# Performance work log

Measured on AMD Instinct MI355X. Metric: run time of the kernel, lower is better.

The kernel has to match this reference:

```python
import jax, jax.numpy as jnp
import numpy as np

SEGMENT_LENGTHS = (2048, 4096, 8192)
DILATION_RATES = (1, 2, 4)
NUM_HEADS = 12
EMBED_DIM = 768
B, N = 2, 8192


def setup_inputs() -> dict:
    key = jax.random.key(0)
    ks = jax.random.split(key, 11)
    E = EMBED_DIM
    return {
        "query": jax.random.normal(ks[0], (B, N, E), jnp.float32),
        "key": jax.random.normal(ks[1], (B, N, E), jnp.float32),
        "value": jax.random.normal(ks[2], (B, N, E), jnp.float32),
        "Wq": jax.random.normal(ks[3], (E, E), jnp.float32) * (E ** -0.5),
        "bq": jax.random.normal(ks[4], (E,), jnp.float32) * 0.02,
        "Wk": jax.random.normal(ks[5], (E, E), jnp.float32) * (E ** -0.5),
        "bk": jax.random.normal(ks[6], (E,), jnp.float32) * 0.02,
        "Wv": jax.random.normal(ks[7], (E, E), jnp.float32) * (E ** -0.5),
        "bv": jax.random.normal(ks[8], (E,), jnp.float32) * 0.02,
        "Wo": jax.random.normal(ks[9], (E, E), jnp.float32) * (E ** -0.5),
        "bo": jax.random.normal(ks[10], (E,), jnp.float32) * 0.02,
    }


def _dilated_attention(q, k, v):
    # q, k, v: [b, n, h, d]
    b, n, h, d = q.shape
    num_groups = len(DILATION_RATES)
    g = h // num_groups  # heads per dilation group
    scale = float(1.0 / np.sqrt(d))  # xformers default softmax scale
    out = jnp.zeros_like(q)
    for i, (r, s) in enumerate(zip(DILATION_RATES, SEGMENT_LENGTHS)):
        off = i % r
        hmin, hmax = i * g, (i + 1) * g
        nseg = n // s
        # gather: [b, nseg, s/r, g, d]
        qg = q.reshape(b, nseg, s, h, d)[:, :, off::r, hmin:hmax, :]
        kg = k.reshape(b, nseg, s, h, d)[:, :, off::r, hmin:hmax, :]
        vg = v.reshape(b, nseg, s, h, d)[:, :, off::r, hmin:hmax, :]
        scores = jnp.einsum("bnqhd,bnkhd->bnhqk", qg, kg) * scale
        attn = jax.nn.softmax(scores, axis=-1)
        x = jnp.einsum("bnhqk,bnkhd->bnqhd", attn, vg)
        out = (
            out.reshape(b, nseg, s, h, d)
            .at[:, :, off::r, hmin:hmax, :]
            .add(x)
            .reshape(b, n, h, d)
        )
    # faithful to original: normalize by sum over the sequence dimension
    return out / jnp.sum(out, axis=1, keepdims=True)


def reference(query, key, value, Wq, bq, Wk, bk, Wv, bv, Wo, bo):
    b, n, e = query.shape
    h = NUM_HEADS
    d = e // h
    q = (query @ Wq.T + bq).reshape(b, n, h, d)
    k = (key @ Wk.T + bk).reshape(b, n, h, d)
    v = (value @ Wv.T + bv).reshape(b, n, h, d)
    x = _dilated_attention(q, k, v)
    x = x.reshape(b, n, e)
    return x @ Wo.T + bo
```

## Files before the change

### kernel.cpp

```cpp
#include <hip/hip_runtime.h>
#include <hip/hip_bf16.h>
#include <cmath>
#include <cstdint>

#define B_ 2
#define N_ 8192
#define H_ 12
#define D_ 64
#define E_ 768
#define M_ (B_*N_)

typedef __attribute__((ext_vector_type(8))) short short8;
typedef __attribute__((ext_vector_type(4))) short short4v;
typedef __attribute__((ext_vector_type(4))) float float4v;

__device__ inline short f2b(float f) {
  union { float f; unsigned u; } x; x.f = f;
  unsigned r = (x.u + 0x7fffu + ((x.u >> 16) & 1u)) >> 16;
  return (short)r;
}
__device__ inline float b2f(short s) {
  union { unsigned u; float f; } x; x.u = ((unsigned)(unsigned short)s) << 16;
  return x.f;
}
__device__ inline void split2(float f, short& h, short& l) {
  h = f2b(f);
  l = f2b(f - b2f(h));
}
__device__ inline unsigned pack_trunc(float a, float b) {
  return (__float_as_uint(b) & 0xffff0000u) | (__float_as_uint(a) >> 16);
}

#define MFMA(a, b, c) __builtin_amdgcn_mfma_f32_16x16x32_bf16((a), (b), (c), 0, 0, 0)

#define GLOAD_LDS16(g, l) \
  __builtin_amdgcn_global_load_lds((const __attribute__((address_space(1))) void*)(g), \
      (__attribute__((address_space(3))) void*)(l), 16, 0, 0)

__global__ __launch_bounds__(256) void split_kernel(const float* __restrict__ src,
    short* __restrict__ hi, short* __restrict__ lo, int count4)
{
  int i = blockIdx.x * 256 + threadIdx.x;
  if (i >= count4) return;
  float4v t = ((const float4v*)src)[i];
  short4v h4, l4; short hh, ll;
  split2(t.x, hh, ll); h4.x = hh; l4.x = ll;
  split2(t.y, hh, ll); h4.y = hh; l4.y = ll;
  split2(t.z, hh, ll); h4.z = hh; l4.z = ll;
  split2(t.w, hh, ll); h4.w = hh; l4.w = ll;
  ((short4v*)hi)[i] = h4;
  ((short4v*)lo)[i] = l4;
}

__global__ __launch_bounds__(256) void split_w4(
    const float* __restrict__ w0, const float* __restrict__ w1,
    const float* __restrict__ w2, const float* __restrict__ w3,
    short* __restrict__ planes)
{
  int which = blockIdx.y;
  const float* src = which == 0 ? w0 : which == 1 ? w1 : which == 2 ? w2 : w3;
  short* hi = planes + (size_t)(2 * which) * (E_ * E_);
  short* lo = planes + (size_t)(2 * which + 1) * (E_ * E_);
  int i = blockIdx.x * 256 + threadIdx.x;
  if (i >= E_ * E_ / 4) return;
  float4v t = ((const float4v*)src)[i];
  short4v h4, l4; short hh, ll;
  split2(t.x, hh, ll); h4.x = hh; l4.x = ll;
  split2(t.y, hh, ll); h4.y = hh; l4.y = ll;
  split2(t.z, hh, ll); h4.z = hh; l4.z = ll;
  split2(t.w, hh, ll); h4.w = hh; l4.w = ll;
  ((short4v*)hi)[i] = h4;
  ((short4v*)lo)[i] = l4;
}

__global__ __launch_bounds__(256) void inv_kernel(const float* __restrict__ sums,
    float* __restrict__ inv)
{
  int i = blockIdx.x * 256 + threadIdx.x;
  if (i < B_ * E_) inv[i] = 1.0f / sums[i];
}

__global__ __launch_bounds__(256) void prep_out(const float* __restrict__ attn,
    const float* __restrict__ inv, short* __restrict__ xnh, short* __restrict__ xnl)
{
  size_t e4 = ((size_t)blockIdx.x * 256 + threadIdx.x) * 4;
  int e = (int)(e4 % E_);
  int b = (int)(e4 / ((size_t)E_ * N_));
  float4v a = *(const float4v*)(attn + e4);
  float4v iv = *(const float4v*)(inv + (size_t)b * E_ + e);
  a *= iv;
  short4v h4, l4; short hh, ll;
  split2(a.x, hh, ll); h4.x = hh; l4.x = ll;
  split2(a.y, hh, ll); h4.y = hh; l4.y = ll;
  split2(a.z, hh, ll); h4.z = hh; l4.z = ll;
  split2(a.w, hh, ll); h4.w = hh; l4.w = ll;
  *(short4v*)&xnh[e4] = h4;
  *(short4v*)&xnl[e4] = l4;
}

template<bool OUT_PAIR>
__global__ __launch_bounds__(256) void gemm_dma(
    const short* __restrict__ Ah, const short* __restrict__ Al,
    const short* __restrict__ Wh, const short* __restrict__ Wl,
    const float* __restrict__ bias, void* __restrict__ OutH, short* __restrict__ OutL)
{
  __shared__ short Ash[4096], Asl[4096], Wsh[4096], Wsl[4096];
  const int tid = threadIdx.x;
  const int m0 = blockIdx.y * 128;
  const int n0 = blockIdx.x * 128;
  const int w = tid >> 6, lane = tid & 63, quad = lane >> 4, l16 = lane & 15;
  const int wr = w >> 1, wc = w & 1;
  const int cq = (l16 >> 1) & 3;
  const int dmarow = lane >> 2;
  const int dmacc = (((lane & 3) ^ ((lane >> 3) & 3))) * 8;

  float4v acc[4][4];
#pragma unroll
  for (int a = 0; a < 4; ++a)
#pragma unroll
    for (int c = 0; c < 4; ++c) acc[a][c] = (float4v)0.0f;

  for (int kt = 0; kt < 24; ++kt) {
    const int k0 = kt * 32;
#pragma unroll
    for (int i = 0; i < 2; ++i) {
      int c = w * 2 + i;
      int ldso = c * 512 + lane * 8;
      size_t ga = (size_t)(m0 + c * 16 + dmarow) * E_ + k0 + dmacc;
      size_t gw = (size_t)(n0 + c * 16 + dmarow) * E_ + k0 + dmacc;
      GLOAD_LDS16(Ah + ga, &Ash[ldso]);
      GLOAD_LDS16(Al + ga, &Asl[ldso]);
      GLOAD_LDS16(Wh + gw, &Wsh[ldso]);
      GLOAD_LDS16(Wl + gw, &Wsl[ldso]);
    }
    __syncthreads();

    short8 afh[4], afl[4], bfh[4], bfl[4];
#pragma unroll
    for (int rt = 0; rt < 4; ++rt) {
      int ao = (wr * 64 + rt * 16 + l16) * 32 + (quad ^ cq) * 8;
      afh[rt] = *(const short8*)&Ash[ao];
      afl[rt] = *(const short8*)&Asl[ao];
      int wo = (wc * 64 + rt * 16 + l16) * 32 + (quad ^ cq) * 8;
      bfh[rt] = *(const short8*)&Wsh[wo];
      bfl[rt] = *(const short8*)&Wsl[wo];
    }
#pragma unroll
    for (int rt = 0; rt < 4; ++rt)
#pragma unroll
      for (int ct = 0; ct < 4; ++ct) {
        float4v a = acc[rt][ct];
        a = MFMA(afh[rt], bfh[ct], a);
        a = MFMA(afh[rt], bfl[ct], a);
        a = MFMA(afl[rt], bfh[ct], a);
        acc[rt][ct] = a;
      }
    __syncthreads();
  }

#pragma unroll
  for (int ct = 0; ct < 4; ++ct) {
    int n = n0 + wc * 64 + ct * 16 + l16;
    float bv = bias[n];
#pragma unroll
    for (int rt = 0; rt < 4; ++rt) {
#pragma unroll
      for (int i = 0; i < 4; ++i) {
        int m = m0 + wr * 64 + rt * 16 + quad * 4 + i;
        float v = acc[rt][ct][i] + bv;
        if constexpr (OUT_PAIR) {
          short hh, ll; split2(v, hh, ll);
          ((short*)OutH)[(size_t)m * E_ + n] = hh;
          OutL[(size_t)m * E_ + n] = ll;
        } else {
          ((float*)OutH)[(size_t)m * E_ + n] = v;
        }
      }
    }
  }
}

__device__ __host__ inline int hoff_of(int g, int hg) {
  return g == 0 ? hg * 8192 : (g == 1 ? 32768 + hg * 4096 : 49152 + hg * 2048);
}

__global__ __launch_bounds__(256) void transpose_v(const short* __restrict__ vh,
    const short* __restrict__ vl, short* __restrict__ vgh, short* __restrict__ vgl)
{
  __shared__ short Lh[64 * 68], Ll[64 * 68];
  int bid = blockIdx.x;
  int b = 0;
  if (bid >= 896) { b = 1; bid -= 896; }
  int g, hg, tile;
  if (bid < 512)      { g = 0; hg = bid >> 7; tile = bid & 127; }
  else if (bid < 768) { g = 1; hg = (bid - 512) >> 6; tile = (bid - 512) & 63; }
  else                { g = 2; hg = (bid - 768) >> 5; tile = (bid - 768) & 31; }
  const int h = g * 4 + hg, r = 1 << g, off = g;
  const int ext = 8192 >> g;
  const int jj0 = tile * 64, seg = jj0 >> 11, j0 = jj0 & 2047;
  const int n0 = seg * (2048 << g) + off + j0 * r;
  const int tid = threadIdx.x;

#pragma unroll
  for (int p = 0; p < 2; ++p) {
    int c = tid + p * 256;
    int jr = c >> 3, c8 = (c & 7) * 8;
    size_t gsrc = ((size_t)(b * N_ + n0 + jr * r) * H_ + h) * D_ + c8;
    *(short8*)&Lh[jr * 68 + c8] = *(const short8*)(vh + gsrc);
    *(short8*)&Ll[jr * 68 + c8] = *(const short8*)(vl + gsrc);
  }
  __syncthreads();
  size_t basebh = ((size_t)b * 57344 + hoff_of(g, hg)) * 64;
#pragma unroll
  for (int p = 0; p < 2; ++p) {
    int c = tid + p * 256;
    int dd = c >> 3, jc = (c & 7) * 8;
    short8 oh, ol;
#pragma unroll
    for (int u = 0; u < 8; ++u) {
      oh[u] = Lh[(jc + u) * 68 + dd];
      ol[u] = Ll[(jc + u) * 68 + dd];
    }
    size_t gdst = basebh + (size_t)dd * ext + jj0 + jc;
    *(short8*)(vgh + gdst) = oh;
    *(short8*)(vgl + gdst) = ol;
  }
}

__global__ __launch_bounds__(256) void attn_kernel(
    const short* __restrict__ qh, const short* __restrict__ ql,
    const short* __restrict__ kh, const short* __restrict__ kl,
    const short* __restrict__ vgh, const short* __restrict__ vgl,
    float* __restrict__ attn_out, float* __restrict__ sums)
{
  __shared__ short Ksh[32 * 72], Ksl[32 * 72];
  __shared__ short Vth[64 * 40], Vtl[64 * 40];
  __shared__ short Psh[4][32 * 40], Psl[4][32 * 40];

  int bid = blockIdx.x;
  int g, t;
  if (bid < 512)      { g = 0; t = bid; }
  else if (bid < 768) { g = 1; t = bid - 512; }
  else                { g = 2; t = bid - 768; }
  const int qtile = t & 15; t >>= 4;
  const int hg = t & 3; t >>= 2;
  const int nseg = 4 >> g;
  const int seg = t & (nseg - 1);
  const int b = t / nseg;
  const int r = 1 << g;
  const int off = g;
  const int h = g * 4 + hg;
  const int segbase = seg * (2048 << g);
  const int ext = 8192 >> g;

  const int tid = threadIdx.x;
  const int w = tid >> 6, lane = tid & 63, quad = lane >> 4, l16 = lane & 15;

  const size_t vbase = ((size_t)b * 57344 + hoff_of(g, hg)) * 64 + (size_t)seg * 2048;

  if (g > 0) {
#pragma unroll
    for (int res0 = 1; res0 < 4; ++res0) {
      if (res0 >= r) break;
      int res = (off + res0) & (r - 1);
      for (int c = 0; c < 8; ++c) {
        int idx = tid + c * 256;
        int jl = idx >> 4, d0 = (idx & 15) * 4;
        int pos = segbase + res + (qtile * 128 + jl) * r;
        *(float4v*)(attn_out + ((size_t)(b * N_ + pos) * H_ + h) * D_ + d0) = (float4v)0.f;
      }
    }
  }

  short8 qfh[2][2], qfl[2][2];
#pragma unroll
  for (int qt = 0; qt < 2; ++qt) {
    int j = qtile * 128 + w * 32 + qt * 16 + l16;
    int pos = segbase + off + j * r;
    size_t base = ((size_t)(b * N_ + pos) * H_ + h) * D_;
#pragma unroll
    for (int ks = 0; ks < 2; ++ks) {
      qfh[qt][ks] = *(const short8*)(qh + base + ks * 32 + quad * 8);
      qfl[qt][ks] = *(const short8*)(ql + base + ks * 32 + quad * 8);
    }
  }

  float4v o[4][2];
  float mrow[2], lrow[2];
#pragma unroll
  for (int dt = 0; dt < 4; ++dt)
#pragma unroll
    for (int qt = 0; qt < 2; ++qt) o[dt][qt] = (float4v)0.0f;
  mrow[0] = mrow[1] = -INFINITY;
  lrow[0] = lrow[1] = 0.f;

  for (int kt = 0; kt < 64; ++kt) {
    {
      int row = tid >> 3, c8 = (tid & 7) * 8;
      int posk = segbase + off + (kt * 32 + row) * r;
      size_t gb = ((size_t)(b * N_ + posk) * H_ + h) * D_ + c8;
      *(short8*)&Ksh[row * 72 + c8] = *(const short8*)(kh + gb);
      *(short8*)&Ksl[row * 72 + c8] = *(const short8*)(kl + gb);
      int dd = tid >> 2, kvc = (tid & 3) * 8;
      size_t vb = vbase + (size_t)dd * ext + kt * 32 + kvc;
      *(short8*)&Vth[dd * 40 + kvc] = *(const short8*)(vgh + vb);
      *(short8*)&Vtl[dd * 40 + kvc] = *(const short8*)(vgl + vb);
    }
    __syncthreads();

    float4v sc[2][2];
#pragma unroll
    for (int kvt = 0; kvt < 2; ++kvt) {
      const int kb = (kvt * 16 + l16) * 72 + quad * 8;
      short8 ah0 = *(const short8*)&Ksh[kb];
      short8 ah1 = *(const short8*)&Ksh[kb + 32];
      short8 al0 = *(const short8*)&Ksl[kb];
      short8 al1 = *(const short8*)&Ksl[kb + 32];
#pragma unroll
      for (int qt = 0; qt < 2; ++qt) {
        float4v a = (float4v)0.0f;
        a = MFMA(ah0, qfh[qt][0], a); a = MFMA(ah1, qfh[qt][1], a);
        a = MFMA(ah0, qfl[qt][0], a); a = MFMA(ah1, qfl[qt][1], a);
        a = MFMA(al0, qfh[qt][0], a); a = MFMA(al1, qfh[qt][1], a);
        sc[qt][kvt] = a * 0.125f;
      }
    }

#pragma unroll
    for (int qt = 0; qt < 2; ++qt) {
      float mx = sc[qt][0][0];
#pragma unroll
      for (int kvt = 0; kvt < 2; ++kvt)
#pragma unroll
        for (int i = 0; i < 4; ++i) mx = fmaxf(mx, sc[qt][kvt][i]);
      mx = fmaxf(mx, __shfl_xor(mx, 16, 64));
      mx = fmaxf(mx, __shfl_xor(mx, 32, 64));
      if (__any(mx > mrow[qt])) {
        float mnew = fmaxf(mrow[qt], mx);
        float alpha = __expf(mrow[qt] - mnew);
        mrow[qt] = mnew;
        lrow[qt] *= alpha;
#pragma unroll
        for (int dt = 0; dt < 4; ++dt) o[dt][qt] *= alpha;
      }
      float rs = 0.f;
#pragma unroll
      for (int kvt = 0; kvt < 2; ++kvt)
#pragma unroll
        for (int i = 0; i < 4; ++i) {
          float p = __expf(sc[qt][kvt][i] - mrow[qt]);
          sc[qt][kvt][i] = p;
          rs += p;
        }
      rs += __shfl_xor(rs, 16, 64);
      rs += __shfl_xor(rs, 32, 64);
      lrow[qt] += rs;

#pragma unroll
      for (int kvt = 0; kvt < 2; ++kvt)
#pragma unroll
        for (int c = 0; c < 2; ++c) {
          float pa = sc[qt][kvt][2 * c], pb = sc[qt][kvt][2 * c + 1];
          unsigned ua = __float_as_uint(pa), ub = __float_as_uint(pb);
          float la = pa - __uint_as_float(ua & 0xffff0000u);
          float lb = pb - __uint_as_float(ub & 0xffff0000u);
          int ad = (qt * 16 + l16) * 40 + kvt * 16 + quad * 4 + 2 * c;
          *(unsigned*)&Psh[w][ad] = (ub & 0xffff0000u) | (ua >> 16);
          *(unsigned*)&Psl[w][ad] = pack_trunc(la, lb);
        }
    }

    short8 pfh[2], pfl[2];
#pragma unroll
    for (int qt = 0; qt < 2; ++qt) {
      pfh[qt] = *(const short8*)&Psh[w][(qt * 16 + l16) * 40 + quad * 8];
      pfl[qt] = *(const short8*)&Psl[w][(qt * 16 + l16) * 40 + quad * 8];
    }
#pragma unroll
    for (int dt = 0; dt < 4; ++dt) {
      short8 vfh = *(const short8*)&Vth[(dt * 16 + l16) * 40 + quad * 8];
      short8 vfl = *(const short8*)&Vtl[(dt * 16 + l16) * 40 + quad * 8];
#pragma unroll
      for (int qt = 0; qt < 2; ++qt) {
        float4v a = o[dt][qt];
        a = MFMA(vfh, pfh[qt], a);
        a = MFMA(vfh, pfl[qt], a);
        a = MFMA(vfl, pfh[qt], a);
        o[dt][qt] = a;
      }
    }
    __syncthreads();
  }

  float4v sacc[4];
#pragma unroll
  for (int dt = 0; dt < 4; ++dt) sacc[dt] = (float4v)0.0f;
#pragma unroll
  for (int qt = 0; qt < 2; ++qt) {
    float inv_l = 1.0f / lrow[qt];
    int j = qtile * 128 + w * 32 + qt * 16 + l16;
    int pos = segbase + off + j * r;
    float* dst = attn_out + ((size_t)(b * N_ + pos) * H_ + h) * D_;
#pragma unroll
    for (int dt = 0; dt < 4; ++dt) {
      float4v v = o[dt][qt] * inv_l;
      *(float4v*)(dst + dt * 16 + quad * 4) = v;
      sacc[dt] += v;
    }
  }
#pragma unroll
  for (int dt = 0; dt < 4; ++dt) {
#pragma unroll
    for (int i = 0; i < 4; ++i) {
      float x = sacc[dt][i];
      x += __shfl_xor(x, 1, 64);
      x += __shfl_xor(x, 2, 64);
      x += __shfl_xor(x, 4, 64);
      x += __shfl_xor(x, 8, 64);
      if (l16 == 0)
        atomicAdd(&sums[(size_t)b * E_ + h * D_ + dt * 16 + quad * 4 + i], x);
    }
  }
}

extern "C" void kernel_launch(void* const* d_in, const int* in_sizes, int n_in,
                              void* d_out, int out_size, void* d_ws, size_t ws_size,
                              hipStream_t stream)
{
  const float* query = (const float*)d_in[0];
  const float* key_  = (const float*)d_in[1];
  const float* value = (const float*)d_in[2];
  const float* Wq = (const float*)d_in[3];
  const float* bq = (const float*)d_in[4];
  const float* Wk = (const float*)d_in[5];
  const float* bk = (const float*)d_in[6];
  const float* Wv = (const float*)d_in[7];
  const float* bv = (const float*)d_in[8];
  const float* Wo = (const float*)d_in[9];
  const float* bo = (const float*)d_in[10];

  char* ws = (char*)d_ws;
  const size_t szbf = (size_t)M_ * E_ * 2;
  const size_t szvg = (size_t)2 * 57344 * 64 * 2;
  const size_t szw  = (size_t)E_ * E_ * 2;
  short* qh_ = (short*)(ws);
  short* ql_ = (short*)(ws + 1 * szbf);
  short* kh_ = (short*)(ws + 2 * szbf);
  short* kl_ = (short*)(ws + 3 * szbf);
  short* vh_ = (short*)(ws + 4 * szbf);
  short* vl_ = (short*)(ws + 5 * szbf);
  short* ish = (short*)(ws + 6 * szbf);
  short* isl = (short*)(ws + 7 * szbf);
  short* vgh = (short*)(ws + 6 * szbf);
  short* vgl = (short*)(ws + 6 * szbf + szvg);
  short* wsp = (short*)(ws + 8 * szbf);
  float* sums = (float*)(ws + 8 * szbf + 8 * szw);
  float* attn = (float*)(ws + 4 * szbf);
  float* inv  = (float*)qh_;
  short* xnh = kh_;
  short* xnl = kl_;
  short* wqh = wsp + 0 * (szw / 2), *wql = wsp + 1 * (szw / 2);
  short* wkh = wsp + 2 * (szw / 2), *wkl = wsp + 3 * (szw / 2);
  short* wvh = wsp + 4 * (szw / 2), *wvl = wsp + 5 * (szw / 2);
  short* woh = wsp + 6 * (szw / 2), *wol = wsp + 7 * (szw / 2);

  hipMemsetAsync(sums, 0, (size_t)B_ * E_ * sizeof(float), stream);

  split_w4<<<dim3(576, 4), 256, 0, stream>>>(Wq, Wk, Wv, Wo, wsp);

  const int ac4 = M_ * E_ / 4;
  dim3 gg(6, 128), gb(256);
  split_kernel<<<12288, 256, 0, stream>>>(query, ish, isl, ac4);
  gemm_dma<true><<<gg, gb, 0, stream>>>(ish, isl, wqh, wql, bq, qh_, ql_);
  split_kernel<<<12288, 256, 0, stream>>>(key_, ish, isl, ac4);
  gemm_dma<true><<<gg, gb, 0, stream>>>(ish, isl, wkh, wkl, bk, kh_, kl_);
  split_kernel<<<12288, 256, 0, stream>>>(value, ish, isl, ac4);
  gemm_dma<true><<<gg, gb, 0, stream>>>(ish, isl, wvh, wvl, bv, vh_, vl_);

  transpose_v<<<1792, 256, 0, stream>>>(vh_, vl_, vgh, vgl);
  attn_kernel<<<896, 256, 0, stream>>>(qh_, ql_, kh_, kl_, vgh, vgl, attn, sums);
  inv_kernel<<<6, 256, 0, stream>>>(sums, inv);
  prep_out<<<12288, 256, 0, stream>>>(attn, inv, xnh, xnl);
  gemm_dma<false><<<gg, gb, 0, stream>>>(xnh, xnl, woh, wol, bo, d_out, nullptr);
}
```

Baseline: 879.8 us.

## Double-buffer K/V tiles with register prefetch and shuffle P via bpermute

The attention kernel now double-buffers K and V tiles in shared memory and prefetches the next-next tile into registers, so global loads overlap with the MFMA work instead of stalling before each iteration. The P-matrix round trip through per-wave shared memory is replaced with ds_bpermute lane shuffles. The scale now folds in log2(e) so exp2f can be used, and s_setprio is raised around the MFMA blocks. These changes add register pressure, and the launch bounds are tightened to request 4 blocks per SM. The loop's final iterations prefetch wrapped tiles (index mod 64), which are loaded but never used.

After: 879.2 us. About the same (-0.1%).

```diff
diff --git a/kernel.cpp b/kernel.cpp
--- a/kernel.cpp
+++ b/kernel.cpp
@@ -227,15 +227,14 @@
   }
 }
 
-__global__ __launch_bounds__(256) void attn_kernel(
+__global__ __launch_bounds__(256, 4) void attn_kernel(
     const short* __restrict__ qh, const short* __restrict__ ql,
     const short* __restrict__ kh, const short* __restrict__ kl,
     const short* __restrict__ vgh, const short* __restrict__ vgl,
     float* __restrict__ attn_out, float* __restrict__ sums)
 {
-  __shared__ short Ksh[32 * 72], Ksl[32 * 72];
-  __shared__ short Vth[64 * 40], Vtl[64 * 40];
-  __shared__ short Psh[4][32 * 40], Psl[4][32 * 40];
+  __shared__ __align__(16) short Ksh[2][32 * 72], Ksl[2][32 * 72];
+  __shared__ __align__(16) short Vth[2][64 * 40], Vtl[2][64 * 40];
 
   int bid = blockIdx.x;
   int g, t;
@@ -255,6 +254,9 @@
 
   const int tid = threadIdx.x;
   const int w = tid >> 6, lane = tid & 63, quad = lane >> 4, l16 = lane & 15;
+  const bool hi5 = (lane & 32) != 0;
+  const int addrA = (l16 + ((lane >> 4) & 1) * 32) << 2;
+  const int addrB = addrA + 64;
 
   const size_t vbase = ((size_t)b * 57344 + hoff_of(g, hg)) * 64 + (size_t)seg * 2048;
 
@@ -285,6 +287,26 @@
     }
   }
 
+  const int srow = tid >> 3, sc8 = (tid & 7) * 8;
+  const int sdd = tid >> 2, skvc = (tid & 3) * 8;
+  size_t gbK = ((size_t)(b * N_ + segbase + off + srow * r) * H_ + h) * D_ + sc8;
+  const size_t stepK = (size_t)32 * r * (H_ * D_);
+  size_t gbV = vbase + (size_t)sdd * ext + skvc;
+
+  short8 rkh, rkl, rvh, rvl;
+#define LOADT(tt) do { \
+    size_t ka_ = gbK + (size_t)(tt) * stepK; \
+    size_t va_ = gbV + (size_t)(tt) * 32; \
+    rkh = *(const short8*)(kh + ka_); rkl = *(const short8*)(kl + ka_); \
+    rvh = *(const short8*)(vgh + va_); rvl = *(const short8*)(vgl + va_); \
+  } while (0)
+#define WRITET(cc) do { \
+    *(short8*)&Ksh[cc][srow * 72 + sc8] = rkh; \
+    *(short8*)&Ksl[cc][srow * 72 + sc8] = rkl; \
+    *(short8*)&Vth[cc][sdd * 40 + skvc] = rvh; \
+    *(short8*)&Vtl[cc][sdd * 40 + skvc] = rvl; \
+  } while (0)
+
   float4v o[4][2];
   float mrow[2], lrow[2];
 #pragma unroll
@@ -294,50 +316,51 @@
   mrow[0] = mrow[1] = -INFINITY;
   lrow[0] = lrow[1] = 0.f;
 
+  LOADT(0);
+  WRITET(0);
+  LOADT(1);
+  __syncthreads();
+  int cur = 0;
+
   for (int kt = 0; kt < 64; ++kt) {
-    {
-      int row = tid >> 3, c8 = (tid & 7) * 8;
-      int posk = segbase + off + (kt * 32 + row) * r;
-      size_t gb = ((size_t)(b * N_ + posk) * H_ + h) * D_ + c8;
-      *(short8*)&Ksh[row * 72 + c8] = *(const short8*)(kh + gb);
-      *(short8*)&Ksl[row * 72 + c8] = *(const short8*)(kl + gb);
-      int dd = tid >> 2, kvc = (tid & 3) * 8;
-      size_t vb = vbase + (size_t)dd * ext + kt * 32 + kvc;
-      *(short8*)&Vth[dd * 40 + kvc] = *(const short8*)(vgh + vb);
-      *(short8*)&Vtl[dd * 40 + kvc] = *(const short8*)(vgl + vb);
-    }
-    __syncthreads();
+    WRITET(cur ^ 1);
+    LOADT((kt + 2) & 63);
+
+    const short* Kc_h = Ksh[cur]; const short* Kc_l = Ksl[cur];
+    const short* Vc_h = Vth[cur]; const short* Vc_l = Vtl[cur];
 
     float4v sc[2][2];
+    __builtin_amdgcn_s_setprio(1);
 #pragma unroll
     for (int kvt = 0; kvt < 2; ++kvt) {
       const int kb = (kvt * 16 + l16) * 72 + quad * 8;
-      short8 ah0 = *(const short8*)&Ksh[kb];
-      short8 ah1 = *(const short8*)&Ksh[kb + 32];
-      short8 al0 = *(const short8*)&Ksl[kb];
-      short8 al1 = *(const short8*)&Ksl[kb + 32];
+      short8 ah0 = *(const short8*)&Kc_h[kb];
+      short8 ah1 = *(const short8*)&Kc_h[kb + 32];
+      short8 al0 = *(const short8*)&Kc_l[kb];
+      short8 al1 = *(const short8*)&Kc_l[kb + 32];
 #pragma unroll
       for (int qt = 0; qt < 2; ++qt) {
         float4v a = (float4v)0.0f;
         a = MFMA(ah0, qfh[qt][0], a); a = MFMA(ah1, qfh[qt][1], a);
         a = MFMA(ah0, qfl[qt][0], a); a = MFMA(ah1, qfl[qt][1], a);
         a = MFMA(al0, qfh[qt][0], a); a = MFMA(al1, qfh[qt][1], a);
-        sc[qt][kvt] = a * 0.125f;
-      }
-    }
-
+        sc[qt][kvt] = a * 0.18033688f;
+      }
+    }
+    __builtin_amdgcn_s_setprio(0);
+
+    short8 pfh[2], pfl[2];
 #pragma unroll
     for (int qt = 0; qt < 2; ++qt) {
-      float mx = sc[qt][0][0];
-#pragma unroll
-      for (int kvt = 0; kvt < 2; ++kvt)
-#pragma unroll
-        for (int i = 0; i < 4; ++i) mx = fmaxf(mx, sc[qt][kvt][i]);
+      float mx = fmaxf(fmaxf(fmaxf(sc[qt][0][0], sc[qt][0][1]),
+                             fmaxf(sc[qt][0][2], sc[qt][0][3])),
+                       fmaxf(fmaxf(sc[qt][1][0], sc[qt][1][1]),
+                             fmaxf(sc[qt][1][2], sc[qt][1][3])));
       mx = fmaxf(mx, __shfl_xor(mx, 16, 64));
       mx = fmaxf(mx, __shfl_xor(mx, 32, 64));
       if (__any(mx > mrow[qt])) {
         float mnew = fmaxf(mrow[qt], mx);
-        float alpha = __expf(mrow[qt] - mnew);
+        float alpha = exp2f(mrow[qt] - mnew);
         mrow[qt] = mnew;
         lrow[qt] *= alpha;
 #pragma unroll
@@ -348,7 +371,7 @@
       for (int kvt = 0; kvt < 2; ++kvt)
 #pragma unroll
         for (int i = 0; i < 4; ++i) {
-          float p = __expf(sc[qt][kvt][i] - mrow[qt]);
+          float p = exp2f(sc[qt][kvt][i] - mrow[qt]);
           sc[qt][kvt][i] = p;
           rs += p;
         }
@@ -356,30 +379,40 @@
       rs += __shfl_xor(rs, 32, 64);
       lrow[qt] += rs;
 
+      unsigned wv_h[2][2], wv_l[2][2];
 #pragma unroll
       for (int kvt = 0; kvt < 2; ++kvt)
 #pragma unroll
         for (int c = 0; c < 2; ++c) {
           float pa = sc[qt][kvt][2 * c], pb = sc[qt][kvt][2 * c + 1];
           unsigned ua = __float_as_uint(pa), ub = __float_as_uint(pb);
+          wv_h[kvt][c] = (ub & 0xffff0000u) | (ua >> 16);
           float la = pa - __uint_as_float(ua & 0xffff0000u);
           float lb = pb - __uint_as_float(ub & 0xffff0000u);
-          int ad = (qt * 16 + l16) * 40 + kvt * 16 + quad * 4 + 2 * c;
-          *(unsigned*)&Psh[w][ad] = (ub & 0xffff0000u) | (ua >> 16);
-          *(unsigned*)&Psl[w][ad] = pack_trunc(la, lb);
+          wv_l[kvt][c] = pack_trunc(la, lb);
         }
-    }
-
-    short8 pfh[2], pfl[2];
-#pragma unroll
-    for (int qt = 0; qt < 2; ++qt) {
-      pfh[qt] = *(const short8*)&Psh[w][(qt * 16 + l16) * 40 + quad * 8];
-      pfl[qt] = *(const short8*)&Psl[w][(qt * 16 + l16) * 40 + quad * 8];
-    }
+      union { unsigned u[4]; short8 s; } oh, ol;
+#pragma unroll
+      for (int j = 0; j < 4; ++j) {
+        int ad = (j < 2) ? addrA : addrB;
+        int c = j & 1;
+        unsigned h0 = (unsigned)__builtin_amdgcn_ds_bpermute(ad, (int)wv_h[0][c]);
+        unsigned h1 = (unsigned)__builtin_amdgcn_ds_bpermute(ad, (int)wv_h[1][c]);
+        unsigned l0 = (unsigned)__builtin_amdgcn_ds_bpermute(ad, (int)wv_l[0][c]);
+        unsigned l1 = (unsigned)__builtin_amdgcn_ds_bpermute(ad, (int)wv_l[1][c]);
+        oh.u[j] = hi5 ? h1 : h0;
+        ol.u[j] = hi5 ? l1 : l0;
+      }
+      pfh[qt] = oh.s;
+      pfl[qt] = ol.s;
+    }
+
+    __builtin_amdgcn_s_setprio(1);
 #pragma unroll
     for (int dt = 0; dt < 4; ++dt) {
-      short8 vfh = *(const short8*)&Vth[(dt * 16 + l16) * 40 + quad * 8];
-      short8 vfl = *(const short8*)&Vtl[(dt * 16 + l16) * 40 + quad * 8];
+      const int vo = (dt * 16 + l16) * 40 + quad * 8;
+      short8 vfh = *(const short8*)&Vc_h[vo];
+      short8 vfl = *(const short8*)&Vc_l[vo];
 #pragma unroll
       for (int qt = 0; qt < 2; ++qt) {
         float4v a = o[dt][qt];
@@ -389,8 +422,13 @@
         o[dt][qt] = a;
       }
     }
+    __builtin_amdgcn_s_setprio(0);
+
     __syncthreads();
-  }
+    cur ^= 1;
+  }
+#undef LOADT
+#undef WRITET
 
   float4v sacc[4];
 #pragma unroll
```

## Software-pipeline attention loop with double-buffered K/V and register-permuted P

Applied to the files above, without the earlier changes.

Restructures the attention inner loop into a two-stage software pipeline. K and V tiles are double-buffered in shared memory and prefetched through registers, and the QK^T of the next tile overlaps the softmax and PV of the current one. P is moved to MFMA operand layout with ds_bpermute instead of a shared-memory round trip. The softmax scale times log2(e) is folded into the Q projection epilogue so exp2f can be used, the row-sum reduction is deferred to the end, and blocks are remapped across groups. It also adds launch bounds and setprio hints, at the cost of more register pressure and more complex control flow.

After: 1.155 ms. +31.2%, slower.

```diff
diff --git a/kernel.cpp b/kernel.cpp
--- a/kernel.cpp
+++ b/kernel.cpp
@@ -102,7 +102,8 @@
 __global__ __launch_bounds__(256) void gemm_dma(
     const short* __restrict__ Ah, const short* __restrict__ Al,
     const short* __restrict__ Wh, const short* __restrict__ Wl,
-    const float* __restrict__ bias, void* __restrict__ OutH, short* __restrict__ OutL)
+    const float* __restrict__ bias, void* __restrict__ OutH, short* __restrict__ OutL,
+    float oscale)
 {
   __shared__ short Ash[4096], Asl[4096], Wsh[4096], Wsl[4096];
   const int tid = threadIdx.x;
@@ -167,7 +168,7 @@
 #pragma unroll
       for (int i = 0; i < 4; ++i) {
         int m = m0 + wr * 64 + rt * 16 + quad * 4 + i;
-        float v = acc[rt][ct][i] + bv;
+        float v = (acc[rt][ct][i] + bv) * oscale;
         if constexpr (OUT_PAIR) {
           short hh, ll; split2(v, hh, ll);
           ((short*)OutH)[(size_t)m * E_ + n] = hh;
@@ -227,17 +228,16 @@
   }
 }
 
-__global__ __launch_bounds__(256) void attn_kernel(
+__global__ __launch_bounds__(256, 4) void attn_kernel(
     const short* __restrict__ qh, const short* __restrict__ ql,
     const short* __restrict__ kh, const short* __restrict__ kl,
     const short* __restrict__ vgh, const short* __restrict__ vgl,
     float* __restrict__ attn_out, float* __restrict__ sums)
 {
-  __shared__ short Ksh[32 * 72], Ksl[32 * 72];
-  __shared__ short Vth[64 * 40], Vtl[64 * 40];
-  __shared__ short Psh[4][32 * 40], Psl[4][32 * 40];
-
-  int bid = blockIdx.x;
+  __shared__ __align__(16) short Ksh[2][32 * 72], Ksl[2][32 * 72];
+  __shared__ __align__(16) short Vth[2][64 * 40], Vtl[2][64 * 40];
+
+  int bid = (blockIdx.x & 7) * 112 + (blockIdx.x >> 3);
   int g, t;
   if (bid < 512)      { g = 0; t = bid; }
   else if (bid < 768) { g = 1; t = bid - 512; }
@@ -255,6 +255,9 @@
 
   const int tid = threadIdx.x;
   const int w = tid >> 6, lane = tid & 63, quad = lane >> 4, l16 = lane & 15;
+  const bool hi5 = (lane & 32) != 0;
+  const int addrA = (l16 + ((lane >> 4) & 1) * 32) << 2;
+  const int addrB = addrA + 64;
 
   const size_t vbase = ((size_t)b * 57344 + hoff_of(g, hg)) * 64 + (size_t)seg * 2048;
 
@@ -285,6 +288,111 @@
     }
   }
 
+  const int srow = tid >> 3, sc8 = (tid & 7) * 8;
+  const int sdd = tid >> 2, skvc = (tid & 3) * 8;
+  size_t gbK = ((size_t)(b * N_ + segbase + off + srow * r) * H_ + h) * D_ + sc8;
+  const size_t stepK = (size_t)32 * r * (H_ * D_);
+  size_t gbV = vbase + (size_t)sdd * ext + skvc;
+
+  short8 rkh, rkl, rvh, rvl;
+#define TCLAMP(tt) ((tt) > 63 ? 63 : (tt))
+#define LOADK(tt) do { size_t ka_ = gbK + (size_t)(tt) * stepK; \
+    rkh = *(const short8*)(kh + ka_); rkl = *(const short8*)(kl + ka_); } while (0)
+#define LOADV(tt) do { size_t va_ = gbV + (size_t)(tt) * 32; \
+    rvh = *(const short8*)(vgh + va_); rvl = *(const short8*)(vgl + va_); } while (0)
+#define WRITEK(cc) do { *(short8*)&Ksh[cc][srow * 72 + sc8] = rkh; \
+    *(short8*)&Ksl[cc][srow * 72 + sc8] = rkl; } while (0)
+#define WRITEV(cc) do { *(short8*)&Vth[cc][sdd * 40 + skvc] = rvh; \
+    *(short8*)&Vtl[cc][sdd * 40 + skvc] = rvl; } while (0)
+
+#define QK_INTO(sdst, kbuf) do { \
+    __builtin_amdgcn_s_setprio(1); \
+    _Pragma("unroll") \
+    for (int kvt = 0; kvt < 2; ++kvt) { \
+      const int kb = (kvt * 16 + l16) * 72 + quad * 8; \
+      short8 ah0 = *(const short8*)&Ksh[kbuf][kb]; \
+      short8 ah1 = *(const short8*)&Ksh[kbuf][kb + 32]; \
+      short8 al0 = *(const short8*)&Ksl[kbuf][kb]; \
+      short8 al1 = *(const short8*)&Ksl[kbuf][kb + 32]; \
+      _Pragma("unroll") \
+      for (int qt = 0; qt < 2; ++qt) { \
+        float4v a = (float4v)0.0f; \
+        a = MFMA(ah0, qfh[qt][0], a); a = MFMA(ah1, qfh[qt][1], a); \
+        a = MFMA(ah0, qfl[qt][0], a); a = MFMA(ah1, qfl[qt][1], a); \
+        a = MFMA(al0, qfh[qt][0], a); a = MFMA(al1, qfh[qt][1], a); \
+        sdst[qt][kvt] = a; \
+      } \
+    } \
+    __builtin_amdgcn_s_setprio(0); \
+  } while (0)
+
+#define SOFTMAX_PV(s, vv) do { \
+    short8 pfh[2], pfl[2]; \
+    _Pragma("unroll") \
+    for (int qt = 0; qt < 2; ++qt) { \
+      float mx = fmaxf(fmaxf(fmaxf(s[qt][0][0], s[qt][0][1]), \
+                             fmaxf(s[qt][0][2], s[qt][0][3])), \
+                       fmaxf(fmaxf(s[qt][1][0], s[qt][1][1]), \
+                             fmaxf(s[qt][1][2], s[qt][1][3]))); \
+      mx = fmaxf(mx, __shfl_xor(mx, 16, 64)); \
+      mx = fmaxf(mx, __shfl_xor(mx, 32, 64)); \
+      if (__any(mx > mrow[qt])) { \
+        float mnew = fmaxf(mrow[qt], mx); \
+        float alpha = exp2f(mrow[qt] - mnew); \
+        mrow[qt] = mnew; lrow[qt] *= alpha; \
+        _Pragma("unroll") for (int dt = 0; dt < 4; ++dt) o[dt][qt] *= alpha; \
+      } \
+      float rs = 0.f; \
+      _Pragma("unroll") \
+      for (int kvt = 0; kvt < 2; ++kvt) \
+        _Pragma("unroll") \
+        for (int i = 0; i < 4; ++i) { \
+          float p = exp2f(s[qt][kvt][i] - mrow[qt]); \
+          s[qt][kvt][i] = p; rs += p; \
+        } \
+      lrow[qt] += rs;   \
+      unsigned wv_h[2][2], wv_l[2][2]; \
+      _Pragma("unroll") \
+      for (int kvt = 0; kvt < 2; ++kvt) \
+        _Pragma("unroll") \
+        for (int c = 0; c < 2; ++c) { \
+          float pa = s[qt][kvt][2 * c], pb = s[qt][kvt][2 * c + 1]; \
+          unsigned ua = __float_as_uint(pa), ub = __float_as_uint(pb); \
+          wv_h[kvt][c] = (ub & 0xffff0000u) | (ua >> 16); \
+          float la = pa - __uint_as_float(ua & 0xffff0000u); \
+          float lb = pb - __uint_as_float(ub & 0xffff0000u); \
+          wv_l[kvt][c] = pack_trunc(la, lb); \
+        } \
+      union { unsigned u[4]; short8 sv; } oh_, ol_; \
+      _Pragma("unroll") \
+      for (int j = 0; j < 4; ++j) { \
+        int ad = (j < 2) ? addrA : addrB; int c = j & 1; \
+        unsigned h0 = (unsigned)__builtin_amdgcn_ds_bpermute(ad, (int)wv_h[0][c]); \
+        unsigned h1 = (unsigned)__builtin_amdgcn_ds_bpermute(ad, (int)wv_h[1][c]); \
+        unsigned l0 = (unsigned)__builtin_amdgcn_ds_bpermute(ad, (int)wv_l[0][c]); \
+        unsigned l1 = (unsigned)__builtin_amdgcn_ds_bpermute(ad, (int)wv_l[1][c]); \
+        oh_.u[j] = hi5 ? h1 : h0; ol_.u[j] = hi5 ? l1 : l0; \
+      } \
+      pfh[qt] = oh_.sv; pfl[qt] = ol_.sv; \
+    } \
+    __builtin_amdgcn_s_setprio(1); \
+    _Pragma("unroll") \
+    for (int dt = 0; dt < 4; ++dt) { \
+      const int vo = (dt * 16 + l16) * 40 + quad * 8; \
+      short8 vfh = *(const short8*)&Vth[vv][vo]; \
+      short8 vfl = *(const short8*)&Vtl[vv][vo]; \
+      _Pragma("unroll") \
+      for (int qt = 0; qt < 2; ++qt) { \
+        float4v a = o[dt][qt]; \
+        a = MFMA(vfh, pfh[qt], a); \
+        a = MFMA(vfh, pfl[qt], a); \
+        a = MFMA(vfl, pfh[qt], a); \
+        o[dt][qt] = a; \
+      } \
+    } \
+    __builtin_amdgcn_s_setprio(0); \
+  } while (0)
+
   float4v o[4][2];
   float mrow[2], lrow[2];
 #pragma unroll
@@ -294,109 +402,47 @@
   mrow[0] = mrow[1] = -INFINITY;
   lrow[0] = lrow[1] = 0.f;
 
-  for (int kt = 0; kt < 64; ++kt) {
-    {
-      int row = tid >> 3, c8 = (tid & 7) * 8;
-      int posk = segbase + off + (kt * 32 + row) * r;
-      size_t gb = ((size_t)(b * N_ + posk) * H_ + h) * D_ + c8;
-      *(short8*)&Ksh[row * 72 + c8] = *(const short8*)(kh + gb);
-      *(short8*)&Ksl[row * 72 + c8] = *(const short8*)(kl + gb);
-      int dd = tid >> 2, kvc = (tid & 3) * 8;
-      size_t vb = vbase + (size_t)dd * ext + kt * 32 + kvc;
-      *(short8*)&Vth[dd * 40 + kvc] = *(const short8*)(vgh + vb);
-      *(short8*)&Vtl[dd * 40 + kvc] = *(const short8*)(vgl + vb);
-    }
+  float4v sA[2][2], sB[2][2];
+
+  LOADK(0); LOADV(0);
+  WRITEK(0); WRITEV(0);
+  LOADK(1);
+  __syncthreads();
+  WRITEK(1);
+  QK_INTO(sA, 0);
+  LOADK(2); LOADV(1);
+  __syncthreads();
+
+  for (int u = 0; u < 32; ++u) {
+    const int kt = 2 * u;
+    WRITEK(0);
+    WRITEV(1);
+    LOADK(TCLAMP(kt + 3)); LOADV(TCLAMP(kt + 2));
+    QK_INTO(sB, 1);
+    SOFTMAX_PV(sA, 0);
     __syncthreads();
-
-    float4v sc[2][2];
-#pragma unroll
-    for (int kvt = 0; kvt < 2; ++kvt) {
-      const int kb = (kvt * 16 + l16) * 72 + quad * 8;
-      short8 ah0 = *(const short8*)&Ksh[kb];
-      short8 ah1 = *(const short8*)&Ksh[kb + 32];
-      short8 al0 = *(const short8*)&Ksl[kb];
-      short8 al1 = *(const short8*)&Ksl[kb + 32];
-#pragma unroll
-      for (int qt = 0; qt < 2; ++qt) {
-        float4v a = (float4v)0.0f;
-        a = MFMA(ah0, qfh[qt][0], a); a = MFMA(ah1, qfh[qt][1], a);
-        a = MFMA(ah0, qfl[qt][0], a); a = MFMA(ah1, qfl[qt][1], a);
-        a = MFMA(al0, qfh[qt][0], a); a = MFMA(al1, qfh[qt][1], a);
-        sc[qt][kvt] = a * 0.125f;
-      }
-    }
-
-#pragma unroll
-    for (int qt = 0; qt < 2; ++qt) {
-      float mx = sc[qt][0][0];
-#pragma unroll
-      for (int kvt = 0; kvt < 2; ++kvt)
-#pragma unroll
-        for (int i = 0; i < 4; ++i) mx = fmaxf(mx, sc[qt][kvt][i]);
-      mx = fmaxf(mx, __shfl_xor(mx, 16, 64));
-      mx = fmaxf(mx, __shfl_xor(mx, 32, 64));
-      if (__any(mx > mrow[qt])) {
-        float mnew = fmaxf(mrow[qt], mx);
-        float alpha = __expf(mrow[qt] - mnew);
-        mrow[qt] = mnew;
-        lrow[qt] *= alpha;
-#pragma unroll
-        for (int dt = 0; dt < 4; ++dt) o[dt][qt] *= alpha;
-      }
-      float rs = 0.f;
-#pragma unroll
-      for (int kvt = 0; kvt < 2; ++kvt)
-#pragma unroll
-        for (int i = 0; i < 4; ++i) {
-          float p = __expf(sc[qt][kvt][i] - mrow[qt]);
-          sc[qt][kvt][i] = p;
-          rs += p;
-        }
-      rs += __shfl_xor(rs, 16, 64);
-      rs += __shfl_xor(rs, 32, 64);
-      lrow[qt] += rs;
-
-#pragma unroll
-      for (int kvt = 0; kvt < 2; ++kvt)
-#pragma unroll
-        for (int c = 0; c < 2; ++c) {
-          float pa = sc[qt][kvt][2 * c], pb = sc[qt][kvt][2 * c + 1];
-          unsigned ua = __float_as_uint(pa), ub = __float_as_uint(pb);
-          float la = pa - __uint_as_float(ua & 0xffff0000u);
-          float lb = pb - __uint_as_float(ub & 0xffff0000u);
-          int ad = (qt * 16 + l16) * 40 + kvt * 16 + quad * 4 + 2 * c;
-          *(unsigned*)&Psh[w][ad] = (ub & 0xffff0000u) | (ua >> 16);
-          *(unsigned*)&Psl[w][ad] = pack_trunc(la, lb);
-        }
-    }
-
-    short8 pfh[2], pfl[2];
-#pragma unroll
-    for (int qt = 0; qt < 2; ++qt) {
-      pfh[qt] = *(const short8*)&Psh[w][(qt * 16 + l16) * 40 + quad * 8];
-      pfl[qt] = *(const short8*)&Psl[w][(qt * 16 + l16) * 40 + quad * 8];
-    }
-#pragma unroll
-    for (int dt = 0; dt < 4; ++dt) {
-      short8 vfh = *(const short8*)&Vth[(dt * 16 + l16) * 40 + quad * 8];
-      short8 vfl = *(const short8*)&Vtl[(dt * 16 + l16) * 40 + quad * 8];
-#pragma unroll
-      for (int qt = 0; qt < 2; ++qt) {
-        float4v a = o[dt][qt];
-        a = MFMA(vfh, pfh[qt], a);
-        a = MFMA(vfh, pfl[qt], a);
-        a = MFMA(vfl, pfh[qt], a);
-        o[dt][qt] = a;
-      }
-    }
+    WRITEK(1);
+    WRITEV(0);
+    LOADK(TCLAMP(kt + 4)); LOADV(TCLAMP(kt + 3));
+    QK_INTO(sA, 0);
+    SOFTMAX_PV(sB, 1);
     __syncthreads();
   }
+#undef TCLAMP
+#undef LOADK
+#undef LOADV
+#undef WRITEK
+#undef WRITEV
+#undef QK_INTO
+#undef SOFTMAX_PV
 
   float4v sacc[4];
 #pragma unroll
   for (int dt = 0; dt < 4; ++dt) sacc[dt] = (float4v)0.0f;
 #pragma unroll
   for (int qt = 0; qt < 2; ++qt) {
+    lrow[qt] += __shfl_xor(lrow[qt], 16, 64);
+    lrow[qt] += __shfl_xor(lrow[qt], 32, 64);
     float inv_l = 1.0f / lrow[qt];
     int j = qtile * 128 + w * 32 + qt * 16 + l16;
     int pos = segbase + off + j * r;
@@ -470,16 +516,17 @@
 
   const int ac4 = M_ * E_ / 4;
   dim3 gg(6, 128), gb(256);
+  const float qscale = 0.18033688f;
   split_kernel<<<12288, 256, 0, stream>>>(query, ish, isl, ac4);
-  gemm_dma<true><<<gg, gb, 0, stream>>>(ish, isl, wqh, wql, bq, qh_, ql_);
+  gemm_dma<true><<<gg, gb, 0, stream>>>(ish, isl, wqh, wql, bq, qh_, ql_, qscale);
   split_kernel<<<12288, 256, 0, stream>>>(key_, ish, isl, ac4);
-  gemm_dma<true><<<gg, gb, 0, stream>>>(ish, isl, wkh, wkl, bk, kh_, kl_);
+  gemm_dma<true><<<gg, gb, 0, stream>>>(ish, isl, wkh, wkl, bk, kh_, kl_, 1.0f);
   split_kernel<<<12288, 256, 0, stream>>>(value, ish, isl, ac4);
-  gemm_dma<true><<<gg, gb, 0, stream>>>(ish, isl, wvh, wvl, bv, vh_, vl_);
+  gemm_dma<true><<<gg, gb, 0, stream>>>(ish, isl, wvh, wvl, bv, vh_, vl_, 1.0f);
 
   transpose_v<<<1792, 256, 0, stream>>>(vh_, vl_, vgh, vgl);
   attn_kernel<<<896, 256, 0, stream>>>(qh_, ql_, kh_, kl_, vgh, vgl, attn, sums);
   inv_kernel<<<6, 256, 0, stream>>>(sums, inv);
   prep_out<<<12288, 256, 0, stream>>>(attn, inv, xnh, xnl);
-  gemm_dma<false><<<gg, gb, 0, stream>>>(xnh, xnl, woh, wol, bo, d_out, nullptr);
-}
+  gemm_dma<false><<<gg, gb, 0, stream>>>(xnh, xnl, woh, wol, bo, d_out, nullptr, 1.0f);
+}
```
